# Kernel tuning notes

Measured on AMD Instinct MI355X. Metric: run time of the kernel, lower is better.

Reference implementation:

```python
import jax, jax.numpy as jnp
import numpy as np

NMS_PRE_MAXSIZE = 4096
NMS_POST_MAXSIZE = 512
NMS_THRESH = 0.7


def setup_inputs() -> dict:
    key = jax.random.key(0)
    k1, k2, k3, k4, k5 = jax.random.split(key, 5)
    B, N, C = 4, 32768, 3
    # realistic 3D boxes: (x, y, z, dx, dy, dz, heading)
    xy = jax.random.uniform(k1, (B, N, 2), dtype=jnp.float32) * 70.0
    z = jax.random.uniform(k2, (B, N, 1), dtype=jnp.float32) * 4.0 - 2.0
    sizes = jax.random.uniform(k3, (B, N, 3), dtype=jnp.float32) * 3.0 + 1.0
    heading = jax.random.uniform(k4, (B, N, 1), dtype=jnp.float32) * 6.2832 - 3.1416
    batch_box_preds = jnp.concatenate([xy, z, sizes, heading], axis=-1)  # (B,N,7)
    batch_cls_preds = jax.random.uniform(k5, (B, N, C), dtype=jnp.float32)  # (B,N,3)
    return {"batch_box_preds": batch_box_preds, "batch_cls_preds": batch_cls_preds}


def _nms_single(boxes, scores, labels):
    # boxes (N,7), scores (N,), labels (N,) int32
    top_s, idx = jax.lax.top_k(scores, NMS_PRE_MAXSIZE)   # sort desc, keep pre-maxsize
    b = boxes[idx]                                        # (PRE,7)
    l = labels[idx]
    # BEV axis-aligned IoU (reference surrogate for the rotated-BEV CUDA IoU kernel)
    x, y, dx, dy = b[:, 0], b[:, 1], b[:, 3], b[:, 4]
    x1, x2 = x - 0.5 * dx, x + 0.5 * dx
    y1, y2 = y - 0.5 * dy, y + 0.5 * dy
    area = dx * dy
    ix = jnp.maximum(0.0, jnp.minimum(x2[:, None], x2[None, :]) - jnp.maximum(x1[:, None], x1[None, :]))
    iy = jnp.maximum(0.0, jnp.minimum(y2[:, None], y2[None, :]) - jnp.maximum(y1[:, None], y1[None, :]))
    inter = ix * iy
    iou = jax.lax.stop_gradient(inter / (area[:, None] + area[None, :] - inter + 1e-6))

    ar = jnp.arange(NMS_PRE_MAXSIZE)

    def body(i, keep):
        sup = (iou[i] > NMS_THRESH) & (ar > i) & keep[i]
        return keep & ~sup

    keep = jax.lax.fori_loop(0, NMS_PRE_MAXSIZE, body, jnp.ones(NMS_PRE_MAXSIZE, bool))

    # pack first NMS_POST_MAXSIZE kept boxes into fixed-size zero-padded outputs
    rank = jnp.cumsum(keep) - 1
    valid = keep & (rank < NMS_POST_MAXSIZE)
    pos = jnp.where(valid, rank, NMS_POST_MAXSIZE)  # invalid -> scratch row
    rois = jnp.zeros((NMS_POST_MAXSIZE + 1, 7), b.dtype).at[pos].set(b)[:NMS_POST_MAXSIZE]
    sc = jnp.zeros((NMS_POST_MAXSIZE + 1,), top_s.dtype).at[pos].set(top_s)[:NMS_POST_MAXSIZE]
    lb = jnp.zeros((NMS_POST_MAXSIZE + 1,), jnp.int32).at[pos].set(l)[:NMS_POST_MAXSIZE]
    return rois, sc, lb


def reference(batch_box_preds, batch_cls_preds):
    # per-box max score / argmax class (torch.max(cls_preds, dim=1) per sample)
    roi_scores_all = jnp.max(batch_cls_preds, axis=-1)                 # (B,N)
    roi_labels_all = jnp.argmax(batch_cls_preds, axis=-1).astype(jnp.int32)
    rois, roi_scores, roi_labels = jax.vmap(_nms_single)(batch_box_preds, roi_scores_all, roi_labels_all)
    return rois, roi_scores, roi_labels + 1  # labels shifted by +1 as in proposal_layer
```

## Files before the change

kernel.cpp:

```cpp
#include <hip/hip_runtime.h>
#include <stdint.h>

#define BB 4
#define NN 32768
#define PRE 4096
#define POST 512
#define NMS_TH 0.7f
#define MIDCAP 8192
#define KCAP 576
#define LROWS 1024

typedef unsigned long long u64;
typedef unsigned int u32;

__device__ __forceinline__ u32 orderable(float f) {
  u32 u = __float_as_uint(f);
  return (u & 0x80000000u) ? ~u : (u | 0x80000000u);
}
__device__ __forceinline__ float unorderable(u32 o) {
  u32 u = (o & 0x80000000u) ? (o & 0x7fffffffu) : ~o;
  return __uint_as_float(u);
}
__device__ __forceinline__ u32 bucket_of(float s) {
  u32 v = (u32)(s * 2147483648.0f);
  u32 bk = v >> 20;
  return bk > 2047u ? 2047u : bk;
}
__device__ __forceinline__ u64 readlane64(u64 v, int l) {
  u32 lo = (u32)__builtin_amdgcn_readlane((int)(u32)v, l);
  u32 hi = (u32)__builtin_amdgcn_readlane((int)(u32)(v >> 32), l);
  return ((u64)hi << 32) | lo;
}
__device__ __forceinline__ bool iou_fast(float4 a, float aa, float4 b, float ba, float& mm) {
  float ix = fminf(a.z, b.z) - fmaxf(a.x, b.x); ix = fmaxf(0.0f, ix);
  float iy = fminf(a.w, b.w) - fmaxf(a.y, b.y); iy = fmaxf(0.0f, iy);
  float inter = ix * iy;
  float denom = ((aa + ba) - inter) + 1e-6f;
  float t = 0.7f * denom;
  mm = fminf(mm, fabsf(inter - t) - 2e-5f * t);
  return inter > t;
}
__device__ __forceinline__ bool iou_exact(float4 a, float aa, float4 b, float ba) {
  float ix = fminf(a.z, b.z) - fmaxf(a.x, b.x); ix = fmaxf(0.0f, ix);
  float iy = fminf(a.w, b.w) - fmaxf(a.y, b.y); iy = fmaxf(0.0f, iy);
  float inter = ix * iy;
  float denom = ((aa + ba) - inter) + 1e-6f;
  return (inter / denom) > NMS_TH;
}

__global__ __launch_bounds__(256) void score_hist_kernel(const float* __restrict__ cls,
                                                         int* __restrict__ labels,
                                                         u64* __restrict__ keys,
                                                         u32* __restrict__ histP) {
  __shared__ u32 lh[2048];
  for (int t = threadIdx.x; t < 2048; t += 256) lh[t] = 0;
  __syncthreads();
  int t4 = blockIdx.x * 256 + threadIdx.x;
  int base4 = t4 * 4;
  const float4* c4 = (const float4*)(cls + (size_t)t4 * 12);
  float4 va = c4[0], vb = c4[1], vc = c4[2];
  float v[12] = {va.x, va.y, va.z, va.w, vb.x, vb.y, vb.z, vb.w, vc.x, vc.y, vc.z, vc.w};
  u64 ks[4]; int ls[4];
#pragma unroll
  for (int p = 0; p < 4; ++p) {
    float s = v[3 * p]; int l = 0;
    if (v[3 * p + 1] > s) { s = v[3 * p + 1]; l = 1; }
    if (v[3 * p + 2] > s) { s = v[3 * p + 2]; l = 2; }
    int n = (base4 + p) & (NN - 1);
    ks[p] = ((u64)orderable(s) << 32) | (u32)(~(u32)n);
    ls[p] = l;
    atomicAdd(&lh[bucket_of(s)], 1u);
  }
  *(ulonglong2*)(keys + base4) = make_ulonglong2(ks[0], ks[1]);
  *(ulonglong2*)(keys + base4 + 2) = make_ulonglong2(ks[2], ks[3]);
  *(int4*)(labels + base4) = make_int4(ls[0], ls[1], ls[2], ls[3]);
  __syncthreads();
  u32* myrow = histP + (size_t)blockIdx.x * 2048;
  for (int t = threadIdx.x; t < 2048; t += 256) myrow[t] = lh[t];
}

__global__ __launch_bounds__(256) void select_kernel(const u32* __restrict__ histP,
                                                     u32* __restrict__ selinfo,
                                                     u32* __restrict__ sfxBuf,
                                                     u32* __restrict__ cursor,
                                                     u32* __restrict__ cnt_mid) {
  __shared__ u32 sfx[2048];
  int b = blockIdx.x;
  if (threadIdx.x == 0) cnt_mid[b] = 0;
  for (int t = threadIdx.x; t < 2048; t += 256) {
    u32 s = 0;
    const u32* pp = histP + (size_t)(b * 32) * 2048 + t;
#pragma unroll
    for (int j = 0; j < 32; ++j) s += pp[(size_t)j * 2048];
    sfx[t] = s;
  }
  __syncthreads();
  for (int d = 1; d < 2048; d <<= 1) {
    u32 v[8];
#pragma unroll
    for (int i = 0; i < 8; ++i) {
      int t = threadIdx.x + i * 256;
      v[i] = (t + d < 2048) ? sfx[t + d] : 0;
    }
    __syncthreads();
#pragma unroll
    for (int i = 0; i < 8; ++i) sfx[threadIdx.x + i * 256] += v[i];
    __syncthreads();
  }
  for (int t = threadIdx.x; t < 2048; t += 256) {
    u32 above = (t + 1 < 2048) ? sfx[t + 1] : 0;
    sfxBuf[b * 2048 + t] = sfx[t];
    cursor[b * 2048 + t] = above;
    if (above < PRE && sfx[t] >= PRE) { selinfo[b * 2] = (u32)t; selinfo[b * 2 + 1] = above; }
  }
}

__global__ __launch_bounds__(256) void compact_kernel(const u64* __restrict__ keys,
                                                      const u32* __restrict__ selinfo,
                                                      u32* __restrict__ cursor,
                                                      u64* __restrict__ sel, u64* __restrict__ mid,
                                                      u32* __restrict__ cnt_mid) {
  int t4 = blockIdx.x * 256 + threadIdx.x;
  int base4 = t4 * 4;
  int b = base4 >> 15;
  u32 T = selinfo[b * 2];
  ulonglong2 k01 = *(const ulonglong2*)(keys + base4);
  ulonglong2 k23 = *(const ulonglong2*)(keys + base4 + 2);
  u64 kk[4] = {k01.x, k01.y, k23.x, k23.y};
#pragma unroll
  for (int p = 0; p < 4; ++p) {
    u64 key = kk[p];
    u32 bk = bucket_of(unorderable((u32)(key >> 32)));
    if (bk > T) {
      u32 q = atomicAdd(&cursor[b * 2048 + bk], 1u);
      sel[((size_t)b << 12) + q] = key;
    } else if (bk == T) {
      u32 q = atomicAdd(&cnt_mid[b], 1u);
      if (q < MIDCAP) mid[(size_t)b * MIDCAP + q] = key;
    }
  }
}

__global__ __launch_bounds__(64) void bsort_kernel(u64* __restrict__ sel, u64* __restrict__ mid,
                                                   const u32* __restrict__ sfxBuf,
                                                   const u32* __restrict__ selinfo,
                                                   const u32* __restrict__ cnt_mid,
                                                   const float* __restrict__ boxes,
                                                   float4* __restrict__ P,
                                                   float* __restrict__ AR,
                                                   float* __restrict__ topS) {
  int t = blockIdx.x & 2047;
  int b = blockIdx.x >> 11;
  int lane = threadIdx.x;
  u32 T = selinfo[b * 2];
  if ((u32)t < T) return;
  u64* selB = sel + ((size_t)b << 12);
  u32 start, end;
  if ((u32)t == T) {
    u32 C1 = selinfo[b * 2 + 1];
    int need = PRE - (int)C1;
    int M = (int)cnt_mid[b]; if (M > MIDCAP) M = MIDCAP;
    u64* midB = mid + (size_t)b * MIDCAP;
    for (int r = 0; r < need; ++r) {
      u64 best = 0; int bi = -1;
      for (int q = lane; q < M; q += 64) {
        u64 v = midB[q];
        if (v > best) { best = v; bi = q; }
      }
#pragma unroll
      for (int d = 32; d > 0; d >>= 1) {
        u64 ob = __shfl_xor(best, d, 64);
        int oi = __shfl_xor(bi, d, 64);
        if (ob > best) { best = ob; bi = oi; }
      }
      if (lane == 0) selB[C1 + r] = best;
      if (bi >= 0 && lane == (bi & 63)) midB[bi] = 0;
    }
    start = C1; end = PRE;
  } else {
    start = (t < 2047) ? sfxBuf[b * 2048 + t + 1] : 0u;
    end = sfxBuf[b * 2048 + t];
    int n = (int)(end - start);
    if (n > 64) {
      for (int r = 0; r < n - 1; ++r) {
        u64 best = 0; int bi = -1;
        for (int q = r + lane; q < n; q += 64) {
          u64 v = selB[start + q];
          if (v > best) { best = v; bi = q; }
        }
#pragma unroll
        for (int d = 32; d > 0; d >>= 1) {
          u64 ob = __shfl_xor(best, d, 64);
          int oi = __shfl_xor(bi, d, 64);
          if (ob > best) { best = ob; bi = oi; }
        }
        if (lane == 0) {
          u64 tmp = selB[start + r];
          selB[start + r] = best;
          selB[start + bi] = tmp;
        }
      }
    } else if (n > 1) {
      u64 v = (lane < n) ? selB[start + lane] : 0ULL;
#pragma unroll
      for (int k = 2; k <= 64; k <<= 1) {
#pragma unroll
        for (int j = k >> 1; j > 0; j >>= 1) {
          u64 o = __shfl_xor(v, j, 64);
          bool up = ((lane & k) == 0);
          bool first = ((lane & j) == 0);
          u64 mx = v > o ? v : o, mn = v > o ? o : v;
          v = (first == up) ? mx : mn;
        }
      }
      if (lane < n) selB[start + lane] = v;
    }
  }
  __builtin_amdgcn_s_waitcnt(0);
  for (u32 pos = start + lane; pos < end; pos += 64) {
    u64 key = selB[pos];
    u32 n = ~(u32)key;
    const float* bx = boxes + ((size_t)b * NN + n) * 7;
    float x = bx[0], y = bx[1], dx = bx[3], dy = bx[4];
    size_t gidx = ((size_t)b << 12) + pos;
    float4 p;
    p.x = x - 0.5f * dx; p.z = x + 0.5f * dx;
    p.y = y - 0.5f * dy; p.w = y + 0.5f * dy;
    P[gidx] = p;
    AR[gidx] = dx * dy;
    topS[gidx] = unorderable((u32)(key >> 32));
  }
}

__global__ __launch_bounds__(1024, 1) void nms_final_kernel(
    const float4* __restrict__ Pg, const float* __restrict__ ARg,
    const float* __restrict__ topS, const u64* __restrict__ selG,
    const float* __restrict__ boxes, const int* __restrict__ labels,
    float* __restrict__ out) {
  __shared__ float4 ldsP[LROWS];
  __shared__ float ldsAR[LROWS];
  __shared__ float4 keptP[KCAP];
  __shared__ float keptAR[KCAP];
  __shared__ u64 dLDS[64];
  __shared__ u64 kwLDS[64];
  __shared__ u32 supArr[64];
  __shared__ int keptIdx[POST];
  __shared__ u32 knSh, finSh, nGrpSh;
  int b = blockIdx.x;
  int tid = threadIdx.x;
  int wv = tid >> 6, lane = tid & 63;
  size_t pb = (size_t)b << 12;
  ldsP[tid] = Pg[pb + tid];
  ldsAR[tid] = ARg[pb + tid];
  if (tid == 0) knSh = 0;
  if (tid < 64) kwLDS[tid] = 0;
  __syncthreads();
  int gEnd = 0;
  for (int g = 0; g < 64; ++g) {
    gEnd = g + 1;
    int kn0 = (int)knSh;
    int cj = g * 64 + 4 * wv + (lane >> 4);
    float4 cp; float car;
    if (cj < LROWS) { cp = ldsP[cj]; car = ldsAR[cj]; }
    else { cp = Pg[pb + cj]; car = ARg[pb + cj]; }
    bool hit = false; float mm = 1.0f;
    int m = lane & 15;
    for (; m + 48 < kn0; m += 64) {
      hit |= iou_fast(keptP[m], keptAR[m], cp, car, mm);
      hit |= iou_fast(keptP[m + 16], keptAR[m + 16], cp, car, mm);
      hit |= iou_fast(keptP[m + 32], keptAR[m + 32], cp, car, mm);
      hit |= iou_fast(keptP[m + 48], keptAR[m + 48], cp, car, mm);
    }
    for (; m < kn0; m += 16)
      hit |= iou_fast(keptP[m], keptAR[m], cp, car, mm);
    if (__any(mm <= 0.0f)) {
      hit = false;
      for (int m2 = (lane & 15); m2 < kn0; m2 += 16)
        hit |= iou_exact(keptP[m2], keptAR[m2], cp, car);
    }
    u64 bal = __ballot(hit);
    int q = lane >> 4;
    if ((lane & 15) == 0)
      supArr[4 * wv + q] = (((bal >> (16 * q)) & 0xFFFFull) != 0ull) ? 1u : 0u;
    int colj = g * 64 + lane;
    float4 cq; float cqa;
    if (colj < LROWS) { cq = ldsP[colj]; cqa = ldsAR[colj]; }
    else { cq = Pg[pb + colj]; cqa = ARg[pb + colj]; }
#pragma unroll
    for (int rr = 0; rr < 4; ++rr) {
      int rj = g * 64 + 4 * wv + rr;
      float4 rp; float rar;
      if (rj < LROWS) { rp = ldsP[rj]; rar = ldsAR[rj]; }
      else { rp = Pg[pb + rj]; rar = ARg[pb + rj]; }
      float mm2 = 1.0f;
      bool sup = iou_fast(rp, rar, cq, cqa, mm2);
      if (__any(mm2 <= 0.0f)) sup = iou_exact(rp, rar, cq, cqa);
      u64 dw = __ballot(sup);
      if (lane == 0) dLDS[4 * wv + rr] = dw;
    }
    __syncthreads();
    if (wv == 0) {
      u64 d_cur = dLDS[lane];
      u64 sup_word = __ballot(supArr[lane] != 0u);
      u64 aboveMask = ~((2ULL << lane) - 1ULL);
      u64 rem = __ballot((d_cur & aboveMask) != 0ULL);
      if (rem) {
        do {
          int k = __ffsll((long long)rem) - 1;
          rem &= rem - 1;
          if (!((sup_word >> k) & 1ULL))
            sup_word |= readlane64(d_cur, k) & ~((2ULL << k) - 1ULL);
        } while (rem);
      }
      u64 keep = ~sup_word;
      int cnt = __popcll(keep);
      int rank = (int)__popcll(keep & ((1ULL << lane) - 1ULL));
      if ((keep >> lane) & 1ULL) {
        int bi = g * 64 + lane;
        if (bi < LROWS) { keptP[kn0 + rank] = ldsP[bi]; keptAR[kn0 + rank] = ldsAR[bi]; }
        else { keptP[kn0 + rank] = Pg[pb + bi]; keptAR[kn0 + rank] = ARg[pb + bi]; }
      }
      if (lane == 0) { kwLDS[g] = keep; knSh = (u32)(kn0 + cnt); }
    }
    __syncthreads();
    if (knSh >= POST) break;
  }
  if (wv == 0) {
    u64 kw = kwLDS[lane];
    int cnt = __popcll(kw);
    int pfx = cnt;
#pragma unroll
    for (int d = 1; d < 64; d <<= 1) {
      int up = __shfl_up(pfx, d, 64);
      if (lane >= d) pfx += up;
    }
    int total = __shfl(pfx, 63, 64);
    int pos = pfx - cnt;
    while (kw) {
      int t = __ffsll((long long)kw) - 1;
      kw &= kw - 1;
      if (pos < POST) keptIdx[pos] = (lane << 6) + t;
      ++pos;
    }
    if (lane == 0) finSh = (u32)(total < POST ? total : POST);
  }
  __syncthreads();
  int fin = (int)finSh;
  float* outR = out;
  float* outS = out + BB * POST * 7;
  float* outL = outS + BB * POST;
  for (int s = tid; s < POST; s += 1024) {
    int gdx = (b << 9) + s;
    if (s < fin) {
      int i = keptIdx[s];
      u64 key = selG[pb + i];
      u32 n = ~(u32)key;
      size_t src = (size_t)b * NN + n;
      const float* bx = boxes + src * 7;
#pragma unroll
      for (int c = 0; c < 7; ++c) outR[(size_t)gdx * 7 + c] = bx[c];
      outS[gdx] = topS[pb + i];
      outL[gdx] = (float)(labels[src] + 1);
    } else {
#pragma unroll
      for (int c = 0; c < 7; ++c) outR[(size_t)gdx * 7 + c] = 0.0f;
      outS[gdx] = 0.0f;
      outL[gdx] = 1.0f;
    }
  }
  (void)gEnd;
}

extern "C" void kernel_launch(void* const* d_in, const int* in_sizes, int n_in,
                              void* d_out, int out_size, void* d_ws, size_t ws_size,
                              hipStream_t stream) {
  const float* boxes = (const float*)d_in[0];
  const float* cls   = (const float*)d_in[1];
  float* out = (float*)d_out;

  char* p = (char*)d_ws;
  auto take = [&](size_t bytes) { char* r = p; p += (bytes + 255) & ~(size_t)255; return (void*)r; };
  u64*   keys    = (u64*)  take((size_t)BB * NN * 8);
  int*   labels  = (int*)  take((size_t)BB * NN * 4);
  u32*   histP   = (u32*)  take((size_t)BB * 32 * 2048 * 4);
  u32*   selinfo = (u32*)  take((size_t)BB * 2 * 4);
  u32*   sfxBuf  = (u32*)  take((size_t)BB * 2048 * 4);
  u32*   cursor  = (u32*)  take((size_t)BB * 2048 * 4);
  u32*   cnt_mid = (u32*)  take((size_t)BB * 4);
  u64*   sel     = (u64*)  take((size_t)BB * PRE * 8);
  u64*   mid     = (u64*)  take((size_t)BB * MIDCAP * 8);
  float4* Pg     = (float4*)take((size_t)BB * PRE * 16);
  float* ARg     = (float*)take((size_t)BB * PRE * 4);
  float* topS    = (float*)take((size_t)BB * PRE * 4);

  score_hist_kernel<<<BB * NN / 1024, 256, 0, stream>>>(cls, labels, keys, histP);
  select_kernel<<<BB, 256, 0, stream>>>(histP, selinfo, sfxBuf, cursor, cnt_mid);
  compact_kernel<<<BB * NN / 1024, 256, 0, stream>>>(keys, selinfo, cursor, sel, mid, cnt_mid);
  bsort_kernel<<<BB * 2048, 64, 0, stream>>>(sel, mid, sfxBuf, selinfo, cnt_mid,
                                             boxes, Pg, ARg, topS);
  nms_final_kernel<<<BB, 1024, 0, stream>>>(Pg, ARg, topS, sel, boxes, labels, out);
}
```

Baseline: 94.11 us.

## Use spatial bin grid to limit IoU checks against kept boxes

Kept boxes are inserted into an 18x18 LDS grid of center bins, and each candidate scans only bins within a radius derived from the maximum box extent. That extent is computed in the gather kernel via an atomicMax. This avoids comparing each candidate against every kept box, cutting the serial NMS inner loop. If a bin overflows its 16-entry capacity, the kernel falls back to the full scan. The grid assumes the coordinate range of the inputs, so the benefit depends on that spatial distribution.

```diff
diff --git a/kernel.cpp b/kernel.cpp
--- a/kernel.cpp
+++ b/kernel.cpp
@@ -9,9 +9,13 @@
 #define MIDCAP 8192
 #define KCAP 576
 #define LROWS 1024
+#define BGRID 18
+#define BINS (BGRID * BGRID)
+#define BCAP 16
 
 typedef unsigned long long u64;
 typedef unsigned int u32;
+typedef unsigned short u16;
 
 __device__ __forceinline__ u32 orderable(float f) {
   u32 u = __float_as_uint(f);
@@ -46,6 +50,10 @@
   float inter = ix * iy;
   float denom = ((aa + ba) - inter) + 1e-6f;
   return (inter / denom) > NMS_TH;
+}
+__device__ __forceinline__ int bin_coord(float c) {
+  int v = (int)(c * 0.25f);
+  return v < 0 ? 0 : (v > BGRID - 1 ? BGRID - 1 : v);
 }
 
 __global__ __launch_bounds__(256) void score_hist_kernel(const float* __restrict__ cls,
@@ -83,10 +91,11 @@
                                                      u32* __restrict__ selinfo,
                                                      u32* __restrict__ sfxBuf,
                                                      u32* __restrict__ cursor,
-                                                     u32* __restrict__ cnt_mid) {
+                                                     u32* __restrict__ cnt_mid,
+                                                     u32* __restrict__ maxWG) {
   __shared__ u32 sfx[2048];
   int b = blockIdx.x;
-  if (threadIdx.x == 0) cnt_mid[b] = 0;
+  if (threadIdx.x == 0) { cnt_mid[b] = 0; maxWG[b] = 0; }
   for (int t = threadIdx.x; t < 2048; t += 256) {
     u32 s = 0;
     const u32* pp = histP + (size_t)(b * 32) * 2048 + t;
@@ -148,7 +157,8 @@
                                                    const float* __restrict__ boxes,
                                                    float4* __restrict__ P,
                                                    float* __restrict__ AR,
-                                                   float* __restrict__ topS) {
+                                                   float* __restrict__ topS,
+                                                   u32* __restrict__ maxWG) {
   int t = blockIdx.x & 2047;
   int b = blockIdx.x >> 11;
   int lane = threadIdx.x;
@@ -217,6 +227,7 @@
     }
   }
   __builtin_amdgcn_s_waitcnt(0);
+  float wmax = 0.0f;
   for (u32 pos = start + lane; pos < end; pos += 64) {
     u64 key = selB[pos];
     u32 n = ~(u32)key;
@@ -229,54 +240,94 @@
     P[gidx] = p;
     AR[gidx] = dx * dy;
     topS[gidx] = unorderable((u32)(key >> 32));
-  }
+    wmax = fmaxf(wmax, fmaxf(dx, dy));
+  }
+#pragma unroll
+  for (int d = 32; d > 0; d >>= 1) wmax = fmaxf(wmax, __shfl_xor(wmax, d, 64));
+  if (lane == 0 && wmax > 0.0f)
+    atomicMax(&maxWG[b], __float_as_uint(wmax));
 }
 
 __global__ __launch_bounds__(1024, 1) void nms_final_kernel(
     const float4* __restrict__ Pg, const float* __restrict__ ARg,
     const float* __restrict__ topS, const u64* __restrict__ selG,
     const float* __restrict__ boxes, const int* __restrict__ labels,
-    float* __restrict__ out) {
+    const u32* __restrict__ maxWG, float* __restrict__ out) {
   __shared__ float4 ldsP[LROWS];
   __shared__ float ldsAR[LROWS];
   __shared__ float4 keptP[KCAP];
   __shared__ float keptAR[KCAP];
+  __shared__ u16 binList[BINS * BCAP];
+  __shared__ u32 binCnt[BINS];
   __shared__ u64 dLDS[64];
   __shared__ u64 kwLDS[64];
   __shared__ u32 supArr[64];
   __shared__ int keptIdx[POST];
-  __shared__ u32 knSh, finSh, nGrpSh;
+  __shared__ u32 knSh, finSh, ovflSh;
   int b = blockIdx.x;
   int tid = threadIdx.x;
   int wv = tid >> 6, lane = tid & 63;
   size_t pb = (size_t)b << 12;
   ldsP[tid] = Pg[pb + tid];
   ldsAR[tid] = ARg[pb + tid];
-  if (tid == 0) knSh = 0;
+  if (tid < BINS) binCnt[tid] = 0;
+  if (tid == 0) { knSh = 0; ovflSh = 0; }
   if (tid < 64) kwLDS[tid] = 0;
   __syncthreads();
-  int gEnd = 0;
+  float maxW = __uint_as_float(maxWG[b]);
+  int rch = 1 + (int)(maxW * 0.25f);
+  if (rch > BGRID - 1) rch = BGRID - 1;
   for (int g = 0; g < 64; ++g) {
-    gEnd = g + 1;
     int kn0 = (int)knSh;
+    bool ovf = (ovflSh != 0);
     int cj = g * 64 + 4 * wv + (lane >> 4);
     float4 cp; float car;
     if (cj < LROWS) { cp = ldsP[cj]; car = ldsAR[cj]; }
     else { cp = Pg[pb + cj]; car = ARg[pb + cj]; }
+    int cbx = bin_coord((cp.x + cp.z) * 0.5f);
+    int cby = bin_coord((cp.y + cp.w) * 0.5f);
+    int x0 = cbx - rch < 0 ? 0 : cbx - rch, x1 = cbx + rch > BGRID - 1 ? BGRID - 1 : cbx + rch;
+    int y0 = cby - rch < 0 ? 0 : cby - rch, y1 = cby + rch > BGRID - 1 ? BGRID - 1 : cby + rch;
     bool hit = false; float mm = 1.0f;
-    int m = lane & 15;
-    for (; m + 48 < kn0; m += 64) {
-      hit |= iou_fast(keptP[m], keptAR[m], cp, car, mm);
-      hit |= iou_fast(keptP[m + 16], keptAR[m + 16], cp, car, mm);
-      hit |= iou_fast(keptP[m + 32], keptAR[m + 32], cp, car, mm);
-      hit |= iou_fast(keptP[m + 48], keptAR[m + 48], cp, car, mm);
-    }
-    for (; m < kn0; m += 16)
-      hit |= iou_fast(keptP[m], keptAR[m], cp, car, mm);
-    if (__any(mm <= 0.0f)) {
-      hit = false;
-      for (int m2 = (lane & 15); m2 < kn0; m2 += 16)
-        hit |= iou_exact(keptP[m2], keptAR[m2], cp, car);
+    if (kn0 > 0) {
+      if (!ovf) {
+        for (int yy = y0; yy <= y1; ++yy)
+          for (int xx = x0; xx <= x1; ++xx) {
+            int bi = yy * BGRID + xx;
+            int cnt = (int)binCnt[bi];
+            for (int e = lane & 15; e < cnt; e += 16) {
+              int m = binList[bi * BCAP + e];
+              hit |= iou_fast(keptP[m], keptAR[m], cp, car, mm);
+            }
+          }
+      } else {
+        int m = lane & 15;
+        for (; m + 48 < kn0; m += 64) {
+          hit |= iou_fast(keptP[m], keptAR[m], cp, car, mm);
+          hit |= iou_fast(keptP[m + 16], keptAR[m + 16], cp, car, mm);
+          hit |= iou_fast(keptP[m + 32], keptAR[m + 32], cp, car, mm);
+          hit |= iou_fast(keptP[m + 48], keptAR[m + 48], cp, car, mm);
+        }
+        for (; m < kn0; m += 16)
+          hit |= iou_fast(keptP[m], keptAR[m], cp, car, mm);
+      }
+      if (__any(mm <= 0.0f)) {
+        hit = false;
+        if (!ovf) {
+          for (int yy = y0; yy <= y1; ++yy)
+            for (int xx = x0; xx <= x1; ++xx) {
+              int bi = yy * BGRID + xx;
+              int cnt = (int)binCnt[bi];
+              for (int e = lane & 15; e < cnt; e += 16) {
+                int m = binList[bi * BCAP + e];
+                hit |= iou_exact(keptP[m], keptAR[m], cp, car);
+              }
+            }
+        } else {
+          for (int m2 = lane & 15; m2 < kn0; m2 += 16)
+            hit |= iou_exact(keptP[m2], keptAR[m2], cp, car);
+        }
+      }
     }
     u64 bal = __ballot(hit);
     int q = lane >> 4;
@@ -317,8 +368,16 @@
       int rank = (int)__popcll(keep & ((1ULL << lane) - 1ULL));
       if ((keep >> lane) & 1ULL) {
         int bi = g * 64 + lane;
-        if (bi < LROWS) { keptP[kn0 + rank] = ldsP[bi]; keptAR[kn0 + rank] = ldsAR[bi]; }
-        else { keptP[kn0 + rank] = Pg[pb + bi]; keptAR[kn0 + rank] = ARg[pb + bi]; }
+        float4 kp; float ka;
+        if (bi < LROWS) { kp = ldsP[bi]; ka = ldsAR[bi]; }
+        else { kp = Pg[pb + bi]; ka = ARg[pb + bi]; }
+        int kpos = kn0 + rank;
+        keptP[kpos] = kp;
+        keptAR[kpos] = ka;
+        int hb = bin_coord((kp.y + kp.w) * 0.5f) * BGRID + bin_coord((kp.x + kp.z) * 0.5f);
+        u32 slot = atomicAdd(&binCnt[hb], 1u);
+        if (slot < BCAP) binList[hb * BCAP + slot] = (u16)kpos;
+        else { ovflSh = 1; binCnt[hb] = BCAP; }
       }
       if (lane == 0) { kwLDS[g] = keep; knSh = (u32)(kn0 + cnt); }
     }
@@ -368,7 +427,6 @@
       outL[gdx] = 1.0f;
     }
   }
-  (void)gEnd;
 }
 
 extern "C" void kernel_launch(void* const* d_in, const int* in_sizes, int n_in,
@@ -387,6 +445,7 @@
   u32*   sfxBuf  = (u32*)  take((size_t)BB * 2048 * 4);
   u32*   cursor  = (u32*)  take((size_t)BB * 2048 * 4);
   u32*   cnt_mid = (u32*)  take((size_t)BB * 4);
+  u32*   maxWG   = (u32*)  take((size_t)BB * 4);
   u64*   sel     = (u64*)  take((size_t)BB * PRE * 8);
   u64*   mid     = (u64*)  take((size_t)BB * MIDCAP * 8);
   float4* Pg     = (float4*)take((size_t)BB * PRE * 16);
@@ -394,9 +453,9 @@
   float* topS    = (float*)take((size_t)BB * PRE * 4);
 
   score_hist_kernel<<<BB * NN / 1024, 256, 0, stream>>>(cls, labels, keys, histP);
-  select_kernel<<<BB, 256, 0, stream>>>(histP, selinfo, sfxBuf, cursor, cnt_mid);
+  select_kernel<<<BB, 256, 0, stream>>>(histP, selinfo, sfxBuf, cursor, cnt_mid, maxWG);
   compact_kernel<<<BB * NN / 1024, 256, 0, stream>>>(keys, selinfo, cursor, sel, mid, cnt_mid);
   bsort_kernel<<<BB * 2048, 64, 0, stream>>>(sel, mid, sfxBuf, selinfo, cnt_mid,
-                                             boxes, Pg, ARg, topS);
-  nms_final_kernel<<<BB, 1024, 0, stream>>>(Pg, ARg, topS, sel, boxes, labels, out);
-}
+                                             boxes, Pg, ARg, topS, maxWG);
+  nms_final_kernel<<<BB, 1024, 0, stream>>>(Pg, ARg, topS, sel, boxes, labels, maxWG, out);
+}
```

New measurement: 93.77 us. Within noise of the previous version (-0.4%).
